# Kernel optimization log

Hardware: AMD Instinct MI355X
Metric: run time of the kernel (lower is better)

## Reference

```python
import jax, jax.numpy as jnp
import numpy as np

NUM_HEADS = 32
NUM_KV_GROUPS = 8


def _rope(x, cos, sin):
    # x: [B, H, S, hd]; cos/sin: [S_max, hd]
    S, hd = x.shape[2], x.shape[3]
    x1, x2 = x[..., : hd // 2], x[..., hd // 2 :]
    rotated = jnp.concatenate((-x2, x1), axis=-1)
    c = cos[:S][None, None]
    s = sin[:S][None, None]
    return (x * c + rotated * s).astype(x.dtype)


def setup_inputs() -> dict:
    key = jax.random.key(0)
    ks = jax.random.split(key, 8)
    B, S, D = 2, 2048, 2048
    H, G = NUM_HEADS, NUM_KV_GROUPS
    hd = D // H
    scale = 1.0 / np.sqrt(D)
    return {
        "inputs": jax.random.normal(ks[0], (B, S, D), jnp.float32),
        "mask": jnp.zeros((S, S), jnp.bool_),  # note: original masked_fill is not in-place -> mask unused
        "cos": jax.random.uniform(ks[1], (S, hd), jnp.float32),
        "sin": jax.random.uniform(ks[2], (S, hd), jnp.float32),
        "Wq": jax.random.normal(ks[3], (D, H * hd), jnp.float32) * scale,
        "Wk": jax.random.normal(ks[4], (D, G * hd), jnp.float32) * scale,
        "Wv": jax.random.normal(ks[5], (D, G * hd), jnp.float32) * scale,
        "Wo": jax.random.normal(ks[6], (H * hd, H * hd), jnp.float32) * scale,
    }


def reference(inputs, mask, cos, sin, Wq, Wk, Wv, Wo):
    B, S, D = inputs.shape
    H, G = NUM_HEADS, NUM_KV_GROUPS
    hd = Wq.shape[1] // H
    group_size = H // G

    q = (inputs @ Wq).reshape(B, S, H, hd).transpose(0, 2, 1, 3)  # [B,H,S,hd]
    k = (inputs @ Wk).reshape(B, S, G, hd).transpose(0, 2, 1, 3)  # [B,G,S,hd]
    v = (inputs @ Wv).reshape(B, S, G, hd).transpose(0, 2, 1, 3)

    q = _rope(q, cos, sin)
    k = _rope(k, cos, sin)

    k = jnp.repeat(k, group_size, axis=1)  # [B,H,S,hd]
    v = jnp.repeat(v, group_size, axis=1)

    scores = jnp.einsum("bhqd,bhkd->bhqk", q, k)
    # NOTE: original uses non-inplace masked_fill whose result is discarded,
    # so faithfully NO mask is applied.
    attn = jax.nn.softmax(scores / jnp.sqrt(jnp.float32(hd)).astype(scores.dtype), axis=-1)
    ctx = jnp.einsum("bhqk,bhkd->bhqd", attn, v)
    ctx = ctx.transpose(0, 2, 1, 3).reshape(B, S, H * hd)
    return ctx @ Wo
```

## Files before the change

kernel.cpp:

```cpp
#include <hip/hip_runtime.h>
#include <stdint.h>

typedef __attribute__((ext_vector_type(8))) short short8;
typedef __attribute__((ext_vector_type(4))) short short4v;
typedef __attribute__((ext_vector_type(4))) float float4v;
typedef __attribute__((ext_vector_type(2))) unsigned uint2v;

__device__ __forceinline__ float bf2f(short s) {
  union { unsigned u; float f; } x;
  x.u = ((unsigned)(unsigned short)s) << 16;
  return x.f;
}
__device__ __forceinline__ short f2bf(float f) {
  union { float f; unsigned u; } x;
  x.f = f;
  unsigned r = x.u + 0x7fffu + ((x.u >> 16) & 1u);
  return (short)(r >> 16);
}
__device__ __forceinline__ float fexp2(float x) {
#if __has_builtin(__builtin_amdgcn_exp2f)
  return __builtin_amdgcn_exp2f(x);
#else
  float r;
  asm("v_exp_f32 %0, %1" : "=v"(r) : "v"(x));
  return r;
#endif
}
__device__ __forceinline__ void glds16(const void* g, void* l) {
  __builtin_amdgcn_global_load_lds(
      (const __attribute__((address_space(1))) void*)g,
      (__attribute__((address_space(3))) void*)l, 16, 0, 0);
}

__global__ __launch_bounds__(256) void f32_to_bf16(const float* __restrict__ s,
                                                   short* __restrict__ d) {
  const long i = ((long)blockIdx.x * 256 + threadIdx.x) * 8;
  const float4v a = *(const float4v*)&s[i];
  const float4v b = *(const float4v*)&s[i + 4];
  short8 v;
#pragma unroll
  for (int e = 0; e < 4; ++e) { v[e] = f2bf(a[e]); v[e + 4] = f2bf(b[e]); }
  *(short8*)&d[i] = v;
}

__device__ __forceinline__ void transpose_tile(
    const float* __restrict__ src, short* __restrict__ dst, int R, int C,
    int r0, int c0) {
  __shared__ short t[64 * 72];
  const int tid = threadIdx.x;
#pragma unroll
  for (int r = 0; r < 2; ++r) {
    int c = r * 256 + tid;
    int row = c >> 3, col8 = (c & 7) * 8;
    const float4v a = *(const float4v*)&src[(long)(r0 + row) * C + c0 + col8];
    const float4v b = *(const float4v*)&src[(long)(r0 + row) * C + c0 + col8 + 4];
    short8 v;
#pragma unroll
    for (int e = 0; e < 4; ++e) { v[e] = f2bf(a[e]); v[e + 4] = f2bf(b[e]); }
    *(short8*)&t[row * 72 + col8] = v;
  }
  __syncthreads();
#pragma unroll
  for (int r = 0; r < 2; ++r) {
    int c = r * 256 + tid;
    int orow = c >> 3, ocol8 = (c & 7) * 8;
    short8 w;
#pragma unroll
    for (int e = 0; e < 8; ++e) w[e] = t[(ocol8 + e) * 72 + orow];
    *(short8*)&dst[(long)(c0 + orow) * R + r0 + ocol8] = w;
  }
}

__global__ __launch_bounds__(256) void transpose_f2b(
    const float* __restrict__ src, short* __restrict__ dst, int R, int C) {
  transpose_tile(src, dst, R, C, blockIdx.y * 64, blockIdx.x * 64);
}

__global__ __launch_bounds__(256) void wtrans3(
    const float* __restrict__ Wq, const float* __restrict__ Wk,
    const float* __restrict__ Wv, short* __restrict__ WT) {
  const int z = blockIdx.z;
  const float* src = z == 0 ? Wq : (z == 1 ? Wk : Wv);
  const int C = z == 0 ? 2048 : 512;
  if (blockIdx.x * 64 >= C) return;
  short* dst = WT + (z == 0 ? 0 : (z == 1 ? 2048 * 2048 : 2560 * 2048));
  transpose_tile(src, dst, 2048, C, blockIdx.y * 64, blockIdx.x * 64);
}

__global__ __launch_bounds__(256) void vtrans(const short* __restrict__ Y,
                                              short* __restrict__ Vt,
                                              int ld, int col0) {
  const int bg = blockIdx.y;
  const int b = bg >> 3, gk = bg & 7;
  const int s0 = blockIdx.x * 64;
  __shared__ short t[64 * 72];
  const int tid = threadIdx.x;
#pragma unroll
  for (int r = 0; r < 2; ++r) {
    int c = r * 256 + tid;
    int row = c >> 3, col8 = (c & 7) * 8;
    short8 v = *(const short8*)&Y[(long)(b * 2048 + s0 + row) * ld + col0 + gk * 64 + col8];
    *(short8*)&t[row * 72 + col8] = v;
  }
  __syncthreads();
#pragma unroll
  for (int r = 0; r < 2; ++r) {
    int c = r * 256 + tid;
    int d = c >> 3, s8 = (c & 7) * 8;
    short8 w;
#pragma unroll
    for (int e = 0; e < 8; ++e) w[e] = t[(s8 + e) * 72 + d];
    *(short8*)&Vt[((long)bg * 64 + d) * 2048 + s0 + s8] = w;
  }
}

__global__ __launch_bounds__(256) void rope_kernel(
    const short* __restrict__ Y, const float* __restrict__ cosp,
    const float* __restrict__ sinp, short* __restrict__ out,
    int NH, int lgNH, int ld, int col0, float scale) {
  const long tid = (long)blockIdx.x * 256 + threadIdx.x;
  const int d = (int)(tid & 31);
  const long t1 = tid >> 5;
  const int h = (int)(t1 & (NH - 1));
  const long t2 = t1 >> lgNH;
  const int s = (int)(t2 & 2047);
  const int b = (int)(t2 >> 11);
  const long ib = (long)(b * 2048 + s) * ld + col0 + h * 64 + d;
  const float x1 = bf2f(Y[ib]);
  const float x2 = bf2f(Y[ib + 32]);
  const float c1 = cosp[s * 64 + d];
  const float c2 = cosp[s * 64 + d + 32];
  const float s1 = sinp[s * 64 + d];
  const float s2 = sinp[s * 64 + d + 32];
  const long ob = ((long)(b * NH + h) * 2048 + s) * 64 + d;
  out[ob] = f2bf((x1 * c1 - x2 * s1) * scale);
  out[ob + 32] = f2bf((x2 * c2 + x1 * s2) * scale);
}

template <typename OutT>
__global__ __launch_bounds__(256) void gemm_bt(
    const short* __restrict__ A, const short* __restrict__ BT,
    OutT* __restrict__ C, int M, int N, int K) {
  __shared__ short As[128 * 32];
  __shared__ short Bs[128 * 32];
  const int tid = threadIdx.x;
  const int wave = tid >> 6, lane = tid & 63;
  const int g = lane >> 4, lr = lane & 15;
  const int m0 = blockIdx.y * 128, n0 = blockIdx.x * 128;
  const int wr = wave >> 1, wc = wave & 1;

  float4v acc[4][4];
#pragma unroll
  for (int i = 0; i < 4; ++i)
#pragma unroll
    for (int j = 0; j < 4; ++j) acc[i][j] = (float4v)0.f;

  for (int kt = 0; kt < K; kt += 32) {
#pragma unroll
    for (int r = 0; r < 2; ++r) {
      const int cb = r * 256 + wave * 64;
      const int c = cb + lane;
      const int row = c >> 2, kc = c & 3;
      glds16(A + (long)(m0 + row) * K + kt + kc * 8, As + cb * 8);
      glds16(BT + (long)(n0 + row) * K + kt + kc * 8, Bs + cb * 8);
    }
    __syncthreads();
    short8 af[4], bfr[4];
#pragma unroll
    for (int i = 0; i < 4; ++i)
      af[i] = *(const short8*)&As[(wr * 64 + i * 16 + lr) * 32 + g * 8];
#pragma unroll
    for (int j = 0; j < 4; ++j)
      bfr[j] = *(const short8*)&Bs[(wc * 64 + j * 16 + lr) * 32 + g * 8];
#pragma unroll
    for (int i = 0; i < 4; ++i)
#pragma unroll
      for (int j = 0; j < 4; ++j)
        acc[i][j] = __builtin_amdgcn_mfma_f32_16x16x32_bf16(af[i], bfr[j], acc[i][j], 0, 0, 0);
    __syncthreads();
  }

#pragma unroll
  for (int i = 0; i < 4; ++i)
#pragma unroll
    for (int j = 0; j < 4; ++j)
#pragma unroll
      for (int t = 0; t < 4; ++t) {
        const int r = m0 + wr * 64 + i * 16 + g * 4 + t;
        const int cc = n0 + wc * 64 + j * 16 + lr;
        float v = acc[i][j][t];
        if constexpr (sizeof(OutT) == 2)
          C[(long)r * N + cc] = f2bf(v);
        else
          C[(long)r * N + cc] = v;
      }
}

__global__ __launch_bounds__(512, 2) void attn_kernel(
    const short* __restrict__ Qr, const short* __restrict__ Kr,
    const short* __restrict__ Vt, short* __restrict__ Ctx) {
  constexpr int S = 2048;
  const int bh = blockIdx.y;
  const int b = bh >> 5, h = bh & 31;
  const int gk = h >> 2;
  const int q0 = blockIdx.x << 7;
  const int tid = threadIdx.x;
  const int w = tid >> 6, lane = tid & 63;
  const int g = lane >> 4, lr = lane & 15;
  const int b8 = lr & 7;
  const int qrow = w * 16 + lr;

  __shared__ short Ks[128 * 64];
  __shared__ short Vs[64 * 128];
  __shared__ short Ps[128 * 128];

  const short* Qb = Qr + (long)(b * 32 + h) * S * 64;
  const short* KbIt = Kr + (long)(b * 8 + gk) * S * 64;
  const short* VbIt = Vt + (long)(b * 8 + gk) * 64 * S;

  const int ko0 = lr * 64 + ((0 + g) ^ b8) * 8;
  const int ko1 = lr * 64 + ((4 + g) ^ b8) * 8;
  const int jv0 = g ^ b8;
  const int vo0 = lr * 128 + jv0 * 8;
  const int vo1 = lr * 128 + (jv0 ^ 4) * 8;
  int pr[4], pw[8];
#pragma unroll
  for (int ks = 0; ks < 4; ++ks) pr[ks] = qrow * 128 + ((4 * ks + g) ^ b8) * 8;
#pragma unroll
  for (int i = 0; i < 8; ++i)
    pw[i] = qrow * 128 + ((2 * i + (g >> 1)) ^ b8) * 8 + (g & 1) * 4;

  long koff[2], voff[2];
#pragma unroll
  for (int r = 0; r < 2; ++r) {
    const int c = r * 512 + w * 64 + lane;
    const int kv = c >> 3, slot = c & 7;
    koff[r] = (long)kv * 64 + (slot ^ (kv & 7)) * 8;
    const int dd = c >> 4, s16 = c & 15;
    voff[r] = (long)dd * S + ((s16 & 8) | ((s16 & 7) ^ (dd & 7))) * 8;
  }

  short8 qf[2];
  qf[0] = *(const short8*)&Qb[(long)(q0 + qrow) * 64 + g * 8];
  qf[1] = *(const short8*)&Qb[(long)(q0 + qrow) * 64 + 32 + g * 8];

  const short8 ones = (short8)(short)0x3F80;
  float4v lacc = (float4v)0.f;
  float4v oacc[4];
#pragma unroll
  for (int di = 0; di < 4; ++di) oacc[di] = (float4v)0.f;

  for (int it = 0; it < 16; ++it) {
#pragma unroll
    for (int r = 0; r < 2; ++r) {
      const int cb = r * 512 + w * 64;
      glds16(KbIt + koff[r], Ks + cb * 8);
      glds16(VbIt + voff[r], Vs + cb * 8);
    }
    __syncthreads();

    float4v sacc[8];
#pragma unroll
    for (int i = 0; i < 8; ++i) sacc[i] = (float4v)0.f;
#pragma unroll
    for (int i = 0; i < 8; ++i) {
      const short8 a0 = *(const short8*)&Ks[ko0 + i * 1024];
      sacc[i] = __builtin_amdgcn_mfma_f32_16x16x32_bf16(a0, qf[0], sacc[i], 0, 0, 0);
    }
#pragma unroll
    for (int i = 0; i < 8; ++i) {
      const short8 a1 = *(const short8*)&Ks[ko1 + i * 1024];
      sacc[i] = __builtin_amdgcn_mfma_f32_16x16x32_bf16(a1, qf[1], sacc[i], 0, 0, 0);
    }

#pragma unroll
    for (int i = 0; i < 8; ++i) {
      union { float f; unsigned u; } a0, a1, a2, a3;
      a0.f = fexp2(sacc[i][0]);
      a1.f = fexp2(sacc[i][1]);
      a2.f = fexp2(sacc[i][2]);
      a3.f = fexp2(sacc[i][3]);
      const unsigned d0 = __builtin_amdgcn_perm(a1.u + 0x8000u, a0.u + 0x8000u, 0x07060302u);
      const unsigned d1 = __builtin_amdgcn_perm(a3.u + 0x8000u, a2.u + 0x8000u, 0x07060302u);
      *(uint2v*)&Ps[pw[i]] = (uint2v){d0, d1};
    }

#pragma unroll
    for (int ks = 0; ks < 4; ++ks) {
      const short8 pf = *(const short8*)&Ps[pr[ks]];
      const int vbase = (ks & 1) ? vo1 : vo0;
      lacc = __builtin_amdgcn_mfma_f32_16x16x32_bf16(ones, pf, lacc, 0, 0, 0);
#pragma unroll
      for (int di = 0; di < 4; ++di) {
        const short8 vf = *(const short8*)&Vs[vbase + di * 2048 + (ks >> 1) * 64];
        oacc[di] = __builtin_amdgcn_mfma_f32_16x16x32_bf16(vf, pf, oacc[di], 0, 0, 0);
      }
    }
    __syncthreads();
    KbIt += 128 * 64;
    VbIt += 128;
  }

  const float inv = 1.f / lacc[0];

  const int q = q0 + qrow;
#pragma unroll
  for (int di = 0; di < 4; ++di) {
    short4v o;
#pragma unroll
    for (int t = 0; t < 4; ++t) o[t] = f2bf(oacc[di][t] * inv);
    *(short4v*)&Ctx[(long)(b * S + q) * 2048 + h * 64 + di * 16 + g * 4] = o;
  }
}

extern "C" void kernel_launch(void* const* d_in, const int* in_sizes, int n_in,
                              void* d_out, int out_size, void* d_ws, size_t ws_size,
                              hipStream_t stream) {
  (void)in_sizes; (void)n_in; (void)out_size; (void)ws_size;
  const float* X    = (const float*)d_in[0];
  const float* cosp = (const float*)d_in[2];
  const float* sinp = (const float*)d_in[3];
  const float* Wq   = (const float*)d_in[4];
  const float* Wk   = (const float*)d_in[5];
  const float* Wv   = (const float*)d_in[6];
  const float* Wo   = (const float*)d_in[7];
  float* out = (float*)d_out;
  char* ws = (char*)d_ws;

  short* Xb = (short*)(ws + 0);
  short* WT = (short*)(ws + 16777216);
  short* Y  = (short*)(ws + 29360128);
  short* Qr = (short*)(ws + 54525952);
  short* Kr = (short*)(ws + 71303168);
  short* Vt = (short*)(ws + 75497472);

  f32_to_bf16<<<4096, 256, 0, stream>>>(X, Xb);
  wtrans3<<<dim3(32, 32, 3), 256, 0, stream>>>(Wq, Wk, Wv, WT);

  gemm_bt<short><<<dim3(24, 32), 256, 0, stream>>>(Xb, WT, Y, 4096, 3072, 2048);

  transpose_f2b<<<dim3(32, 32), 256, 0, stream>>>(Wo, WT, 2048, 2048);

  rope_kernel<<<16384, 256, 0, stream>>>(Y, cosp, sinp, Qr, 32, 5, 3072, 0, 0.18033688011112043f);
  rope_kernel<<<4096, 256, 0, stream>>>(Y, cosp, sinp, Kr, 8, 3, 3072, 2048, 1.0f);
  vtrans<<<dim3(32, 16), 256, 0, stream>>>(Y, Vt, 3072, 2560);

  attn_kernel<<<dim3(16, 64), 512, 0, stream>>>(Qr, Kr, Vt, Y);

  gemm_bt<float><<<dim3(16, 32), 256, 0, stream>>>(Y, WT, out, 4096, 2048, 2048);
}
```

Measured before the change: 374.7 us.

## Fuse RoPE into QKV GEMM epilogue, double-buffer attention with smaller KV tiles

The QKV GEMM epilogue now applies RoPE and the softmax scale directly and writes Q and K in head-major layout. This removes both rope kernels and the intermediate Y round trip, and V is written to a compact buffer for the transpose. The attention kernel switches to 64-key tiles with double-buffered K/V loads into LDS, explicit vmcnt waits, raw barriers, setprio hints around the MFMA blocks, and launch bounds raised to 6 blocks per CU for occupancy. The GEMM also remaps block IDs for L2 locality. The fused epilogue writes scattered bf16 stores, and the smaller tiles double the number of loop iterations.

```diff
diff --git a/kernel.cpp b/kernel.cpp
--- a/kernel.cpp
+++ b/kernel.cpp
@@ -31,6 +31,7 @@
       (const __attribute__((address_space(1))) void*)g,
       (__attribute__((address_space(3))) void*)l, 16, 0, 0);
 }
+__device__ __forceinline__ void bar() { __builtin_amdgcn_s_barrier(); }
 
 __global__ __launch_bounds__(256) void f32_to_bf16(const float* __restrict__ s,
                                                    short* __restrict__ d) {
@@ -114,40 +115,25 @@
   }
 }
 
-__global__ __launch_bounds__(256) void rope_kernel(
-    const short* __restrict__ Y, const float* __restrict__ cosp,
-    const float* __restrict__ sinp, short* __restrict__ out,
-    int NH, int lgNH, int ld, int col0, float scale) {
-  const long tid = (long)blockIdx.x * 256 + threadIdx.x;
-  const int d = (int)(tid & 31);
-  const long t1 = tid >> 5;
-  const int h = (int)(t1 & (NH - 1));
-  const long t2 = t1 >> lgNH;
-  const int s = (int)(t2 & 2047);
-  const int b = (int)(t2 >> 11);
-  const long ib = (long)(b * 2048 + s) * ld + col0 + h * 64 + d;
-  const float x1 = bf2f(Y[ib]);
-  const float x2 = bf2f(Y[ib + 32]);
-  const float c1 = cosp[s * 64 + d];
-  const float c2 = cosp[s * 64 + d + 32];
-  const float s1 = sinp[s * 64 + d];
-  const float s2 = sinp[s * 64 + d + 32];
-  const long ob = ((long)(b * NH + h) * 2048 + s) * 64 + d;
-  out[ob] = f2bf((x1 * c1 - x2 * s1) * scale);
-  out[ob + 32] = f2bf((x2 * c2 + x1 * s2) * scale);
-}
-
-template <typename OutT>
+template <int MODE>
 __global__ __launch_bounds__(256) void gemm_bt(
     const short* __restrict__ A, const short* __restrict__ BT,
-    OutT* __restrict__ C, int M, int N, int K) {
+    float* __restrict__ Cf, short* __restrict__ Qr, short* __restrict__ Kr,
+    short* __restrict__ YV, const float* __restrict__ cosp,
+    const float* __restrict__ sinp, int M, int N, int K) {
+  (void)M;
   __shared__ short As[128 * 32];
   __shared__ short Bs[128 * 32];
   const int tid = threadIdx.x;
   const int wave = tid >> 6, lane = tid & 63;
   const int g = lane >> 4, lr = lane & 15;
-  const int m0 = blockIdx.y * 128, n0 = blockIdx.x * 128;
   const int wr = wave >> 1, wc = wave & 1;
+
+  const int nbx = gridDim.x;
+  const int nwg = nbx * gridDim.y;
+  const int bid = blockIdx.y * nbx + blockIdx.x;
+  const int nbid = (bid & 7) * (nwg >> 3) + (bid >> 3);
+  const int m0 = (nbid / nbx) << 7, n0 = (nbid % nbx) << 7;
 
   float4v acc[4][4];
 #pragma unroll
@@ -180,26 +166,54 @@
     __syncthreads();
   }
 
-#pragma unroll
-  for (int i = 0; i < 4; ++i)
-#pragma unroll
-    for (int j = 0; j < 4; ++j)
+  if constexpr (MODE == 1) {
+    const int h = (n0 + wc * 64) >> 6;
+#pragma unroll
+    for (int i = 0; i < 4; ++i)
 #pragma unroll
       for (int t = 0; t < 4; ++t) {
         const int r = m0 + wr * 64 + i * 16 + g * 4 + t;
-        const int cc = n0 + wc * 64 + j * 16 + lr;
-        float v = acc[i][j][t];
-        if constexpr (sizeof(OutT) == 2)
-          C[(long)r * N + cc] = f2bf(v);
-        else
-          C[(long)r * N + cc] = v;
+        const int s = r & 2047, bb = r >> 11;
+        if (h < 40) {
+          const float sc = h < 32 ? 0.18033688011112043f : 1.0f;
+          short* base = h < 32
+              ? Qr + ((long)(bb * 32 + h) * 2048 + s) * 64
+              : Kr + ((long)(bb * 8 + (h - 32)) * 2048 + s) * 64;
+          const float* cr = cosp + s * 64;
+          const float* sr = sinp + s * 64;
+#pragma unroll
+          for (int j = 0; j < 2; ++j) {
+            const int d = j * 16 + lr;
+            const float x1 = acc[i][j][t];
+            const float x2 = acc[i][j + 2][t];
+            base[d] = f2bf((x1 * cr[d] - x2 * sr[d]) * sc);
+            base[d + 32] = f2bf((x2 * cr[d + 32] + x1 * sr[d + 32]) * sc);
+          }
+        } else {
+          short* base = YV + ((long)bb * 2048 + s) * 512 + (h - 40) * 64;
+#pragma unroll
+          for (int j = 0; j < 4; ++j) base[j * 16 + lr] = f2bf(acc[i][j][t]);
+        }
       }
-}
-
-__global__ __launch_bounds__(512, 2) void attn_kernel(
+  } else {
+#pragma unroll
+    for (int i = 0; i < 4; ++i)
+#pragma unroll
+      for (int j = 0; j < 4; ++j)
+#pragma unroll
+        for (int t = 0; t < 4; ++t) {
+          const int r = m0 + wr * 64 + i * 16 + g * 4 + t;
+          const int cc = n0 + wc * 64 + j * 16 + lr;
+          Cf[(long)r * N + cc] = acc[i][j][t];
+        }
+  }
+}
+
+__global__ __launch_bounds__(512, 6) void attn_kernel(
     const short* __restrict__ Qr, const short* __restrict__ Kr,
     const short* __restrict__ Vt, short* __restrict__ Ctx) {
   constexpr int S = 2048;
+  constexpr int NIT = 32;
   const int bh = blockIdx.y;
   const int b = bh >> 5, h = bh & 31;
   const int gk = h >> 2;
@@ -210,35 +224,29 @@
   const int b8 = lr & 7;
   const int qrow = w * 16 + lr;
 
-  __shared__ short Ks[128 * 64];
-  __shared__ short Vs[64 * 128];
-  __shared__ short Ps[128 * 128];
+  __shared__ short Ks[2][64 * 64];
+  __shared__ short Vs[2][64 * 64];
+  __shared__ short Ps[128 * 64];
 
   const short* Qb = Qr + (long)(b * 32 + h) * S * 64;
-  const short* KbIt = Kr + (long)(b * 8 + gk) * S * 64;
-  const short* VbIt = Vt + (long)(b * 8 + gk) * 64 * S;
+  const short* Kb = Kr + (long)(b * 8 + gk) * S * 64;
+  const short* Vb = Vt + (long)(b * 8 + gk) * 64 * S;
 
   const int ko0 = lr * 64 + ((0 + g) ^ b8) * 8;
   const int ko1 = lr * 64 + ((4 + g) ^ b8) * 8;
-  const int jv0 = g ^ b8;
-  const int vo0 = lr * 128 + jv0 * 8;
-  const int vo1 = lr * 128 + (jv0 ^ 4) * 8;
-  int pr[4], pw[8];
-#pragma unroll
-  for (int ks = 0; ks < 4; ++ks) pr[ks] = qrow * 128 + ((4 * ks + g) ^ b8) * 8;
-#pragma unroll
-  for (int i = 0; i < 8; ++i)
-    pw[i] = qrow * 128 + ((2 * i + (g >> 1)) ^ b8) * 8 + (g & 1) * 4;
-
-  long koff[2], voff[2];
-#pragma unroll
-  for (int r = 0; r < 2; ++r) {
-    const int c = r * 512 + w * 64 + lane;
-    const int kv = c >> 3, slot = c & 7;
-    koff[r] = (long)kv * 64 + (slot ^ (kv & 7)) * 8;
-    const int dd = c >> 4, s16 = c & 15;
-    voff[r] = (long)dd * S + ((s16 & 8) | ((s16 & 7) ^ (dd & 7))) * 8;
-  }
+  int vo[2], pr[2], pw[4];
+#pragma unroll
+  for (int ks = 0; ks < 2; ++ks) {
+    vo[ks] = lr * 64 + ((ks * 4 + g) ^ b8) * 8;
+    pr[ks] = qrow * 64 + ((ks * 4 + g) ^ b8) * 8;
+  }
+#pragma unroll
+  for (int i = 0; i < 4; ++i)
+    pw[i] = qrow * 64 + ((2 * i + (g >> 1)) ^ b8) * 8 + (g & 1) * 4;
+
+  const int srow = tid >> 3, sl = tid & 7;
+  const long koff = (long)srow * 64 + (sl ^ (srow & 7)) * 8;
+  const long voff = (long)srow * S + (sl ^ (srow & 7)) * 8;
 
   short8 qf[2];
   qf[0] = *(const short8*)&Qb[(long)(q0 + qrow) * 64 + g * 8];
@@ -250,31 +258,39 @@
 #pragma unroll
   for (int di = 0; di < 4; ++di) oacc[di] = (float4v)0.f;
 
-  for (int it = 0; it < 16; ++it) {
-#pragma unroll
-    for (int r = 0; r < 2; ++r) {
-      const int cb = r * 512 + w * 64;
-      glds16(KbIt + koff[r], Ks + cb * 8);
-      glds16(VbIt + voff[r], Vs + cb * 8);
-    }
-    __syncthreads();
-
-    float4v sacc[8];
-#pragma unroll
-    for (int i = 0; i < 8; ++i) sacc[i] = (float4v)0.f;
-#pragma unroll
-    for (int i = 0; i < 8; ++i) {
-      const short8 a0 = *(const short8*)&Ks[ko0 + i * 1024];
+  glds16(Kb + koff, &Ks[0][w * 512]);
+  glds16(Vb + voff, &Vs[0][w * 512]);
+
+  for (int it = 0; it < NIT; ++it) {
+    const int buf = it & 1;
+    if (it + 1 < NIT) {
+      glds16(Kb + (long)(it + 1) * 64 * 64 + koff, &Ks[buf ^ 1][w * 512]);
+      glds16(Vb + (it + 1) * 64 + voff, &Vs[buf ^ 1][w * 512]);
+      asm volatile("s_waitcnt vmcnt(2)" ::: "memory");
+    } else {
+      asm volatile("s_waitcnt vmcnt(0)" ::: "memory");
+    }
+    __builtin_amdgcn_sched_barrier(0);
+    bar();
+
+    float4v sacc[4];
+#pragma unroll
+    for (int i = 0; i < 4; ++i) sacc[i] = (float4v)0.f;
+    __builtin_amdgcn_s_setprio(1);
+#pragma unroll
+    for (int i = 0; i < 4; ++i) {
+      const short8 a0 = *(const short8*)&Ks[buf][ko0 + i * 1024];
       sacc[i] = __builtin_amdgcn_mfma_f32_16x16x32_bf16(a0, qf[0], sacc[i], 0, 0, 0);
     }
 #pragma unroll
-    for (int i = 0; i < 8; ++i) {
-      const short8 a1 = *(const short8*)&Ks[ko1 + i * 1024];
+    for (int i = 0; i < 4; ++i) {
+      const short8 a1 = *(const short8*)&Ks[buf][ko1 + i * 1024];
       sacc[i] = __builtin_amdgcn_mfma_f32_16x16x32_bf16(a1, qf[1], sacc[i], 0, 0, 0);
     }
-
-#pragma unroll
-    for (int i = 0; i < 8; ++i) {
+    __builtin_amdgcn_s_setprio(0);
+
+#pragma unroll
+    for (int i = 0; i < 4; ++i) {
       union { float f; unsigned u; } a0, a1, a2, a3;
       a0.f = fexp2(sacc[i][0]);
       a1.f = fexp2(sacc[i][1]);
@@ -285,20 +301,19 @@
       *(uint2v*)&Ps[pw[i]] = (uint2v){d0, d1};
     }
 
-#pragma unroll
-    for (int ks = 0; ks < 4; ++ks) {
+    __builtin_amdgcn_s_setprio(1);
+#pragma unroll
+    for (int ks = 0; ks < 2; ++ks) {
       const short8 pf = *(const short8*)&Ps[pr[ks]];
-      const int vbase = (ks & 1) ? vo1 : vo0;
       lacc = __builtin_amdgcn_mfma_f32_16x16x32_bf16(ones, pf, lacc, 0, 0, 0);
 #pragma unroll
       for (int di = 0; di < 4; ++di) {
-        const short8 vf = *(const short8*)&Vs[vbase + di * 2048 + (ks >> 1) * 64];
+        const short8 vf = *(const short8*)&Vs[buf][vo[ks] + di * 1024];
         oacc[di] = __builtin_amdgcn_mfma_f32_16x16x32_bf16(vf, pf, oacc[di], 0, 0, 0);
       }
     }
-    __syncthreads();
-    KbIt += 128 * 64;
-    VbIt += 128;
+    __builtin_amdgcn_s_setprio(0);
+    bar();
   }
 
   const float inv = 1.f / lacc[0];
@@ -330,22 +345,23 @@
   short* Xb = (short*)(ws + 0);
   short* WT = (short*)(ws + 16777216);
   short* Y  = (short*)(ws + 29360128);
-  short* Qr = (short*)(ws + 54525952);
-  short* Kr = (short*)(ws + 71303168);
-  short* Vt = (short*)(ws + 75497472);
+  short* Qr = (short*)(ws + 46137344);
+  short* Kr = (short*)(ws + 62914560);
+  short* YV = (short*)(ws + 67108864);
+  short* Vt = (short*)(ws + 71303168);
 
   f32_to_bf16<<<4096, 256, 0, stream>>>(X, Xb);
   wtrans3<<<dim3(32, 32, 3), 256, 0, stream>>>(Wq, Wk, Wv, WT);
 
-  gemm_bt<short><<<dim3(24, 32), 256, 0, stream>>>(Xb, WT, Y, 4096, 3072, 2048);
+  gemm_bt<1><<<dim3(24, 32), 256, 0, stream>>>(
+      Xb, WT, nullptr, Qr, Kr, YV, cosp, sinp, 4096, 3072, 2048);
 
   transpose_f2b<<<dim3(32, 32), 256, 0, stream>>>(Wo, WT, 2048, 2048);
 
-  rope_kernel<<<16384, 256, 0, stream>>>(Y, cosp, sinp, Qr, 32, 5, 3072, 0, 0.18033688011112043f);
-  rope_kernel<<<4096, 256, 0, stream>>>(Y, cosp, sinp, Kr, 8, 3, 3072, 2048, 1.0f);
-  vtrans<<<dim3(32, 16), 256, 0, stream>>>(Y, Vt, 3072, 2560);
+  vtrans<<<dim3(32, 16), 256, 0, stream>>>(YV, Vt, 512, 0);
 
   attn_kernel<<<dim3(16, 64), 512, 0, stream>>>(Qr, Kr, Vt, Y);
 
-  gemm_bt<float><<<dim3(16, 32), 256, 0, stream>>>(Y, WT, out, 4096, 2048, 2048);
-}
+  gemm_bt<2><<<dim3(16, 32), 256, 0, stream>>>(
+      Y, WT, out, nullptr, nullptr, nullptr, nullptr, nullptr, 4096, 2048, 2048);
+}
```

Result: no change. 370.4 us (-1.1%).
